# Kernel tuning notes

Hardware: AMD Instinct MI355X
Metric: run time of the kernel (lower is better)

The kernel has to match this reference:

```python
import jax, jax.numpy as jnp
import numpy as np

N = 50000      # nodes
E = 800000     # edges (before self loops)
F_IN = 128
HID = 32
HEADS = 4
OUT_DIM = 1
NEG_SLOPE = 0.2


def gat_conv(x, edge_src, edge_dst, W, a_src, a_dst, bias):
    """PyG GATConv (concat=True, self-loops already appended to edge lists).
    x: [N, Fin], W: [Fin, H*D], a_src/a_dst: [H, D], bias: [H*D]."""
    H, D = a_src.shape
    h = (x @ W).reshape(N, H, D)                      # [N, H, D]
    alpha_src = jnp.einsum('nhd,hd->nh', h, a_src)    # [N, H]
    alpha_dst = jnp.einsum('nhd,hd->nh', h, a_dst)    # [N, H]
    e = alpha_src[edge_src] + alpha_dst[edge_dst]     # [Et, H]
    e = jnp.where(e > 0, e, NEG_SLOPE * e)            # leaky_relu(0.2)
    # softmax over edges grouped by destination node
    m = jax.ops.segment_max(e, edge_dst, num_segments=N)  # [N, H]
    e = jnp.exp(e - jax.lax.stop_gradient(m)[edge_dst])
    s = jax.ops.segment_sum(e, edge_dst, num_segments=N)  # [N, H]
    alpha = e / (s[edge_dst] + 1e-16)                 # [Et, H]
    msg = h[edge_src] * alpha[:, :, None]             # [Et, H, D]
    out = jax.ops.segment_sum(msg, edge_dst, num_segments=N)  # [N, H, D]
    return out.reshape(N, H * D) + bias


def setup_inputs() -> dict:
    key = jax.random.key(0)
    ks = jax.random.split(key, 16)
    HD = HEADS * HID
    def glorot(k, shape, fan_in):
        return jax.random.normal(k, shape, dtype=jnp.float32) / np.sqrt(fan_in)
    inp = {
        'x': jax.random.normal(ks[0], (N, F_IN), dtype=jnp.float32),
        'edge_index': jax.random.randint(ks[1], (2, E), 0, N, dtype=jnp.int64 if jax.config.jax_enable_x64 else jnp.int32),
        'W1': glorot(ks[2], (F_IN, HD), F_IN),
        'a_src1': glorot(ks[3], (HEADS, HID), HID),
        'a_dst1': glorot(ks[4], (HEADS, HID), HID),
        'b1': jnp.zeros((HD,), dtype=jnp.float32),
        'W2': glorot(ks[5], (HD, HD), HD),
        'a_src2': glorot(ks[6], (HEADS, HID), HID),
        'a_dst2': glorot(ks[7], (HEADS, HID), HID),
        'b2': jnp.zeros((HD,), dtype=jnp.float32),
        'Wc1': glorot(ks[8], (HD, HID), HD),
        'bc1': jnp.zeros((HID,), dtype=jnp.float32),
        'Wc2': glorot(ks[9], (HID, OUT_DIM), HID),
        'bc2': jnp.zeros((OUT_DIM,), dtype=jnp.float32),
    }
    return inp


def reference(x, edge_index, W1, a_src1, a_dst1, b1, W2, a_src2, a_dst2, b2,
              Wc1, bc1, Wc2, bc2):
    # PyG add_self_loops=True: append (i -> i) for every node
    loops = jnp.arange(N, dtype=edge_index.dtype)
    src = jnp.concatenate([edge_index[0], loops])
    dst = jnp.concatenate([edge_index[1], loops])
    h = gat_conv(x, src, dst, W1, a_src1, a_dst1, b1)
    h = jax.nn.relu(h)
    h = gat_conv(h, src, dst, W2, a_src2, a_dst2, b2)
    h = jax.nn.relu(h)
    # classifier (dropout is identity at eval)
    h = h @ Wc1 + bc1
    h = h @ Wc2 + bc2
    return jax.nn.sigmoid(h)
```

## Files before the change

kernel.cpp:

```cpp
#include <hip/hip_runtime.h>
#include <hip/hip_bf16.h>
#include <math.h>

#define NEG_SLOPE 0.2f

__device__ __forceinline__ unsigned short f2bf(float f) {
    unsigned int u = __float_as_uint(f);
    u = (u + 0x7fffu + ((u >> 16) & 1u)) >> 16;
    return (unsigned short)u;
}
__device__ __forceinline__ float bflo(unsigned int p) {
    return __uint_as_float(p << 16);
}
__device__ __forceinline__ float bfhi(unsigned int p) {
    return __uint_as_float(p & 0xffff0000u);
}

__global__ __launch_bounds__(256) void gemm_alpha_kernel(
    const float* __restrict__ X, const float* __restrict__ W,
    const float* __restrict__ a_src, const float* __restrict__ a_dst,
    unsigned short* __restrict__ Hb, float* __restrict__ as_out,
    float* __restrict__ ad_out, int N)
{
    __shared__ float xt[64 * 128];
    int n0 = blockIdx.x * 64;
    int t  = threadIdx.x;

    {
        const float4* src = (const float4*)(X + (size_t)n0 * 128);
        float4* dst = (float4*)xt;
        int rows = N - n0; if (rows > 64) rows = 64;
        int maxv = rows * 32;
        #pragma unroll
        for (int i = 0; i < 8; ++i) {
            int idx = t + i * 256;
            int g = idx < maxv ? idx : maxv - 1;
            dst[idx] = src[g];
        }
    }
    __syncthreads();

    int rg = t >> 5;
    int c  = t & 31;
    int j0 = c * 4;

    float acc[8][4];
    #pragma unroll
    for (int rr = 0; rr < 8; ++rr)
        { acc[rr][0]=0.f; acc[rr][1]=0.f; acc[rr][2]=0.f; acc[rr][3]=0.f; }

    #pragma unroll 2
    for (int k = 0; k < 128; ++k) {
        float4 w = *(const float4*)(W + k * 128 + j0);
        #pragma unroll
        for (int rr = 0; rr < 8; ++rr) {
            float xv = xt[(rg + rr * 8) * 128 + k];
            acc[rr][0] = fmaf(xv, w.x, acc[rr][0]);
            acc[rr][1] = fmaf(xv, w.y, acc[rr][1]);
            acc[rr][2] = fmaf(xv, w.z, acc[rr][2]);
            acc[rr][3] = fmaf(xv, w.w, acc[rr][3]);
        }
    }

    float4 asv = *(const float4*)(a_src + j0);
    float4 adv = *(const float4*)(a_dst + j0);
    int head = c >> 3;
    int wlane = (c & 7) == 0;

    #pragma unroll
    for (int rr = 0; rr < 8; ++rr) {
        float b0 = acc[rr][0], b1 = acc[rr][1], b2 = acc[rr][2], b3 = acc[rr][3];
        int row = n0 + rg + rr * 8;
        bool valid = row < N;
        if (valid) {
            unsigned int lo = (unsigned int)f2bf(b0) | ((unsigned int)f2bf(b1) << 16);
            unsigned int hi = (unsigned int)f2bf(b2) | ((unsigned int)f2bf(b3) << 16);
            *(uint2*)(Hb + (size_t)row * 128 + j0) = make_uint2(lo, hi);
        }
        float ps = b0*asv.x + b1*asv.y + b2*asv.z + b3*asv.w;
        float pd = b0*adv.x + b1*adv.y + b2*adv.z + b3*adv.w;
        ps += __shfl_xor(ps, 1, 64); pd += __shfl_xor(pd, 1, 64);
        ps += __shfl_xor(ps, 2, 64); pd += __shfl_xor(pd, 2, 64);
        ps += __shfl_xor(ps, 4, 64); pd += __shfl_xor(pd, 4, 64);
        if (wlane && valid) {
            as_out[row * 4 + head] = ps;
            ad_out[row * 4 + head] = pd;
        }
    }
}

__global__ __launch_bounds__(256) void zero_int_kernel(int* __restrict__ p, int n)
{
    int i = blockIdx.x * 256 + threadIdx.x;
    if (i < n) p[i] = 0;
}

__global__ __launch_bounds__(256) void count_rank_kernel(
    const int* __restrict__ edst, int E, int Et,
    int* __restrict__ cnt, int* __restrict__ rank)
{
    int e = blockIdx.x * 256 + threadIdx.x;
    if (e >= Et) return;
    int d = (e < E) ? edst[e] : (e - E);
    rank[e] = atomicAdd(&cnt[d], 1);
}

__global__ __launch_bounds__(256) void pos_kernel(
    const int* __restrict__ edst, int E, int Et,
    const int* __restrict__ offs, int* __restrict__ rank)
{
    int e = blockIdx.x * 256 + threadIdx.x;
    if (e >= Et) return;
    int d = (e < E) ? edst[e] : (e - E);
    rank[e] = offs[d] + rank[e];
}

__global__ __launch_bounds__(256) void scan_block_kernel(
    const int* __restrict__ in, int* __restrict__ out,
    int* __restrict__ bsum, int n)
{
    __shared__ int sh[256];
    int i = blockIdx.x * 256 + threadIdx.x;
    int v = (i < n) ? in[i] : 0;
    sh[threadIdx.x] = v;
    __syncthreads();
    #pragma unroll
    for (int off = 1; off < 256; off <<= 1) {
        int t = 0;
        if (threadIdx.x >= off) t = sh[threadIdx.x - off];
        __syncthreads();
        if (threadIdx.x >= off) sh[threadIdx.x] += t;
        __syncthreads();
    }
    if (i < n) out[i] = sh[threadIdx.x] - v;
    if (threadIdx.x == 255) bsum[blockIdx.x] = sh[255];
}

__global__ __launch_bounds__(256) void scan_add_kernel(
    int* __restrict__ offs, const int* __restrict__ bsum, int n)
{
    int i = blockIdx.x * 256 + threadIdx.x;
    if (i < n) offs[i] += bsum[blockIdx.x];
}

__global__ __launch_bounds__(256) void fill_kernel(
    const int* __restrict__ esrc, int E, int Et, int N,
    const int* __restrict__ offs, const int* __restrict__ pos,
    int* __restrict__ csr, int S)
{
    int slice = blockIdx.x >> 3;
    int l8 = blockIdx.x & 7;
    if (slice >= S) return;
    int rlo = (int)(((long long)N * l8) >> 3);
    int rhi = (int)(((long long)N * (l8 + 1)) >> 3);
    int csrLo = offs[rlo];
    int csrHi = (rhi < N) ? offs[rhi] : Et;
    int e0 = (int)((long long)Et * slice / S);
    int e1 = (int)((long long)Et * (slice + 1) / S);
    for (int e = e0 + threadIdx.x; e < e1; e += 256) {
        int p = pos[e];
        if (p >= csrLo && p < csrHi)
            csr[p] = (e < E) ? esrc[e] : (e - E);
    }
}

__global__ __launch_bounds__(128) void cls_vec_kernel(
    const float* __restrict__ Wc1, const float* __restrict__ bc1,
    const float* __restrict__ Wc2, const float* __restrict__ bc2,
    float* __restrict__ v)
{
    int i = threadIdx.x;
    float acc = 0.f;
    #pragma unroll
    for (int j = 0; j < 32; ++j)
        acc = fmaf(Wc1[i * 32 + j], Wc2[j], acc);
    v[i] = acc;
    if (i == 0) {
        float c = bc2[0];
        for (int j = 0; j < 32; ++j)
            c = fmaf(bc1[j], Wc2[j], c);
        v[128] = c;
    }
}

__global__ __launch_bounds__(256) void gat_fused_kernel(
    const unsigned short* __restrict__ Hb, const int* __restrict__ csr,
    const int* __restrict__ offs, const int* __restrict__ cnt,
    const float* __restrict__ as, const float* __restrict__ ad,
    const float* __restrict__ bias, float* __restrict__ out, int N,
    const float* __restrict__ v, float* __restrict__ dcls, int docls)
{
    __shared__ float wtab[4 * 256];
    __shared__ int   stab[4 * 64];

    int t = threadIdx.x;
    int wv = t >> 6;
    int g  = (t >> 4) & 3;
    int q  = t & 15;
    int d = blockIdx.x * 16 + (t >> 4);
    if (d >= N) return;
    int start = offs[d];
    int deg = cnt[d];
    float4 adv = *(const float4*)(ad + d * 4);
    int h = q >> 2;
    int f0 = q * 8;

    float m0 = -INFINITY, m1 = -INFINITY, m2 = -INFINITY, m3 = -INFINITY;
    float s0 = 0.f, s1 = 0.f, s2 = 0.f, s3 = 0.f;
    float acc0=0.f,acc1=0.f,acc2=0.f,acc3=0.f,acc4=0.f,acc5=0.f,acc6=0.f,acc7=0.f;

    const float* wbase = wtab + wv * 256 + g * 4 + h;
    const int*   sbase = stab + wv * 64 + g * 16;

    for (int c0 = 0; c0 < deg; c0 += 16) {
        int rem = deg - c0;
        int len = rem < 16 ? rem : 16;
        bool valid = q < len;
        int sidx = valid ? csr[start + c0 + q] : 0;
        float4 av = *(const float4*)(as + sidx * 4);
        float e0 = av.x + adv.x; e0 = e0 > 0.f ? e0 : NEG_SLOPE * e0;
        float e1 = av.y + adv.y; e1 = e1 > 0.f ? e1 : NEG_SLOPE * e1;
        float e2 = av.z + adv.z; e2 = e2 > 0.f ? e2 : NEG_SLOPE * e2;
        float e3 = av.w + adv.w; e3 = e3 > 0.f ? e3 : NEG_SLOPE * e3;
        if (!valid) { e0 = e1 = e2 = e3 = -INFINITY; }

        float c0m = e0, c1m = e1, c2m = e2, c3m = e3;
        #pragma unroll
        for (int off = 8; off; off >>= 1) {
            c0m = fmaxf(c0m, __shfl_xor(c0m, off, 64));
            c1m = fmaxf(c1m, __shfl_xor(c1m, off, 64));
            c2m = fmaxf(c2m, __shfl_xor(c2m, off, 64));
            c3m = fmaxf(c3m, __shfl_xor(c3m, off, 64));
        }
        float nm0 = fmaxf(m0, c0m), nm1 = fmaxf(m1, c1m);
        float nm2 = fmaxf(m2, c2m), nm3 = fmaxf(m3, c3m);
        float r0 = __expf(m0 - nm0), r1 = __expf(m1 - nm1);
        float r2 = __expf(m2 - nm2), r3 = __expf(m3 - nm3);
        m0 = nm0; m1 = nm1; m2 = nm2; m3 = nm3;

        float w0 = valid ? __expf(e0 - m0) : 0.f;
        float w1 = valid ? __expf(e1 - m1) : 0.f;
        float w2 = valid ? __expf(e2 - m2) : 0.f;
        float w3 = valid ? __expf(e3 - m3) : 0.f;

        float t0 = w0, t1 = w1, t2 = w2, t3 = w3;
        #pragma unroll
        for (int off = 8; off; off >>= 1) {
            t0 += __shfl_xor(t0, off, 64);
            t1 += __shfl_xor(t1, off, 64);
            t2 += __shfl_xor(t2, off, 64);
            t3 += __shfl_xor(t3, off, 64);
        }
        s0 = s0 * r0 + t0; s1 = s1 * r1 + t1;
        s2 = s2 * r2 + t2; s3 = s3 * r3 + t3;
        float rs = h == 0 ? r0 : (h == 1 ? r1 : (h == 2 ? r2 : r3));
        acc0 *= rs; acc1 *= rs; acc2 *= rs; acc3 *= rs;
        acc4 *= rs; acc5 *= rs; acc6 *= rs; acc7 *= rs;

        ((float4*)wtab)[wv * 64 + q * 4 + g] = make_float4(w0, w1, w2, w3);
        stab[wv * 64 + g * 16 + q] = sidx;

        int kk = 0;
        for (; kk + 4 <= len; kk += 4) {
            int sk0 = sbase[kk+0], sk1 = sbase[kk+1];
            int sk2 = sbase[kk+2], sk3 = sbase[kk+3];
            float wa = wbase[(kk+0)*16], wb = wbase[(kk+1)*16];
            float wc = wbase[(kk+2)*16], wd = wbase[(kk+3)*16];
            uint4 p0 = *(const uint4*)(Hb + (size_t)sk0 * 128 + f0);
            uint4 p1 = *(const uint4*)(Hb + (size_t)sk1 * 128 + f0);
            uint4 p2 = *(const uint4*)(Hb + (size_t)sk2 * 128 + f0);
            uint4 p3 = *(const uint4*)(Hb + (size_t)sk3 * 128 + f0);
            acc0 = fmaf(wa, bflo(p0.x), acc0); acc1 = fmaf(wa, bfhi(p0.x), acc1);
            acc2 = fmaf(wa, bflo(p0.y), acc2); acc3 = fmaf(wa, bfhi(p0.y), acc3);
            acc4 = fmaf(wa, bflo(p0.z), acc4); acc5 = fmaf(wa, bfhi(p0.z), acc5);
            acc6 = fmaf(wa, bflo(p0.w), acc6); acc7 = fmaf(wa, bfhi(p0.w), acc7);
            acc0 = fmaf(wb, bflo(p1.x), acc0); acc1 = fmaf(wb, bfhi(p1.x), acc1);
            acc2 = fmaf(wb, bflo(p1.y), acc2); acc3 = fmaf(wb, bfhi(p1.y), acc3);
            acc4 = fmaf(wb, bflo(p1.z), acc4); acc5 = fmaf(wb, bfhi(p1.z), acc5);
            acc6 = fmaf(wb, bflo(p1.w), acc6); acc7 = fmaf(wb, bfhi(p1.w), acc7);
            acc0 = fmaf(wc, bflo(p2.x), acc0); acc1 = fmaf(wc, bfhi(p2.x), acc1);
            acc2 = fmaf(wc, bflo(p2.y), acc2); acc3 = fmaf(wc, bfhi(p2.y), acc3);
            acc4 = fmaf(wc, bflo(p2.z), acc4); acc5 = fmaf(wc, bfhi(p2.z), acc5);
            acc6 = fmaf(wc, bflo(p2.w), acc6); acc7 = fmaf(wc, bfhi(p2.w), acc7);
            acc0 = fmaf(wd, bflo(p3.x), acc0); acc1 = fmaf(wd, bfhi(p3.x), acc1);
            acc2 = fmaf(wd, bflo(p3.y), acc2); acc3 = fmaf(wd, bfhi(p3.y), acc3);
            acc4 = fmaf(wd, bflo(p3.z), acc4); acc5 = fmaf(wd, bfhi(p3.z), acc5);
            acc6 = fmaf(wd, bflo(p3.w), acc6); acc7 = fmaf(wd, bfhi(p3.w), acc7);
        }
        for (; kk < len; ++kk) {
            int sk = sbase[kk];
            float wk = wbase[kk*16];
            uint4 p = *(const uint4*)(Hb + (size_t)sk * 128 + f0);
            acc0 = fmaf(wk, bflo(p.x), acc0); acc1 = fmaf(wk, bfhi(p.x), acc1);
            acc2 = fmaf(wk, bflo(p.y), acc2); acc3 = fmaf(wk, bfhi(p.y), acc3);
            acc4 = fmaf(wk, bflo(p.z), acc4); acc5 = fmaf(wk, bfhi(p.z), acc5);
            acc6 = fmaf(wk, bflo(p.w), acc6); acc7 = fmaf(wk, bfhi(p.w), acc7);
        }
    }

    float sh = h == 0 ? s0 : (h == 1 ? s1 : (h == 2 ? s2 : s3));
    float inv = 1.f / (sh + 1e-16f);
    float4 bA = *(const float4*)(bias + f0);
    float4 bB = *(const float4*)(bias + f0 + 4);
    float o0 = fmaxf(acc0 * inv + bA.x, 0.f);
    float o1 = fmaxf(acc1 * inv + bA.y, 0.f);
    float o2 = fmaxf(acc2 * inv + bA.z, 0.f);
    float o3 = fmaxf(acc3 * inv + bA.w, 0.f);
    float o4 = fmaxf(acc4 * inv + bB.x, 0.f);
    float o5 = fmaxf(acc5 * inv + bB.y, 0.f);
    float o6 = fmaxf(acc6 * inv + bB.z, 0.f);
    float o7 = fmaxf(acc7 * inv + bB.w, 0.f);

    if (!docls) {
        *(float4*)(out + (size_t)d * 128 + f0)     = make_float4(o0, o1, o2, o3);
        *(float4*)(out + (size_t)d * 128 + f0 + 4) = make_float4(o4, o5, o6, o7);
    } else {
        float4 vA = *(const float4*)(v + f0);
        float4 vB = *(const float4*)(v + f0 + 4);
        float part = o0*vA.x + o1*vA.y + o2*vA.z + o3*vA.w
                   + o4*vB.x + o5*vB.y + o6*vB.z + o7*vB.w;
        part += __shfl_xor(part, 1, 64);
        part += __shfl_xor(part, 2, 64);
        part += __shfl_xor(part, 4, 64);
        part += __shfl_xor(part, 8, 64);
        if (q == 0)
            dcls[d] = 1.0f / (1.0f + __expf(-(part + v[128])));
    }
}

extern "C" void kernel_launch(void* const* d_in, const int* in_sizes, int n_in,
                              void* d_out, int out_size, void* d_ws, size_t ws_size,
                              hipStream_t stream)
{
    const float* x      = (const float*)d_in[0];
    const int*   eidx   = (const int*)d_in[1];
    const float* W1     = (const float*)d_in[2];
    const float* a_src1 = (const float*)d_in[3];
    const float* a_dst1 = (const float*)d_in[4];
    const float* b1     = (const float*)d_in[5];
    const float* W2     = (const float*)d_in[6];
    const float* a_src2 = (const float*)d_in[7];
    const float* a_dst2 = (const float*)d_in[8];
    const float* b2     = (const float*)d_in[9];
    const float* Wc1    = (const float*)d_in[10];
    const float* bc1    = (const float*)d_in[11];
    const float* Wc2    = (const float*)d_in[12];
    const float* bc2    = (const float*)d_in[13];

    int N  = in_sizes[0] / 128;
    int E  = in_sizes[1] / 2;
    int Et = E + N;
    const int* esrc = eidx;
    const int* edst = eidx + E;

    char* wsb = (char*)d_ws;
    unsigned short* Hb = (unsigned short*)wsb;  wsb += (size_t)N * 128 * 2;
    float*  f1_buf = (float*)wsb;   wsb += (size_t)N * 128 * 4;
    float*  as_buf = (float*)wsb;   wsb += (size_t)N * 4 * 4;
    float*  ad_buf = (float*)wsb;   wsb += (size_t)N * 4 * 4;
    int*    cnt    = (int*)wsb;     wsb += (size_t)N * 4;
    int*    offs   = (int*)wsb;     wsb += (size_t)N * 4;
    int*    bsum   = (int*)wsb;     wsb += 512 * 4;
    int*    csr    = (int*)wsb;     wsb += (size_t)Et * 4;
    int*    rank   = (int*)wsb;     wsb += (size_t)Et * 4;
    float*  vcls   = (float*)wsb;   wsb += 132 * 4;

    int nbN = (N + 255) / 256;
    int nbE = (Et + 255) / 256;
    int gemmBlocks = (N + 63) / 64;
    int S = 512;

    zero_int_kernel<<<nbN, 256, 0, stream>>>(cnt, N);
    count_rank_kernel<<<nbE, 256, 0, stream>>>(edst, E, Et, cnt, rank);
    scan_block_kernel<<<nbN, 256, 0, stream>>>(cnt, offs, bsum, N);
    scan_block_kernel<<<1, 256, 0, stream>>>(bsum, bsum, &bsum[300], nbN);
    scan_add_kernel<<<nbN, 256, 0, stream>>>(offs, bsum, N);
    pos_kernel<<<nbE, 256, 0, stream>>>(edst, E, Et, offs, rank);
    cls_vec_kernel<<<1, 128, 0, stream>>>(Wc1, bc1, Wc2, bc2, vcls);
    fill_kernel<<<S * 8, 256, 0, stream>>>(esrc, E, Et, N, offs, rank, csr, S);

    gemm_alpha_kernel<<<gemmBlocks, 256, 0, stream>>>(x, W1, a_src1, a_dst1,
                                                      Hb, as_buf, ad_buf, N);
    gat_fused_kernel<<<(N + 15) / 16, 256, 0, stream>>>(Hb, csr, offs, cnt,
        as_buf, ad_buf, b1, f1_buf, N, vcls, (float*)d_out, 0);
    gemm_alpha_kernel<<<gemmBlocks, 256, 0, stream>>>(f1_buf, W2, a_src2, a_dst2,
                                                      Hb, as_buf, ad_buf, N);
    gat_fused_kernel<<<(N + 15) / 16, 256, 0, stream>>>(Hb, csr, offs, cnt,
        as_buf, ad_buf, b2, f1_buf, N, vcls, (float*)d_out, 1);
}
```

Measured before the change: 310.7 us.

## Process 64-edge chunks per destination and unroll the gather loop by eight

Each destination's 16-lane group now handles up to 64 incoming edges per iteration, with every lane scoring four edges. The score max and sum are combined locally before the cross-lane shuffles. This cuts the number of online-softmax rescale and shuffle rounds for typical degrees near 17. The gather loop now issues eight bf16 row loads before accumulating, to keep more memory requests in flight. The cost is more registers for the edge scores and loaded rows, plus a larger shared-memory table, which may lower occupancy.

```diff
diff --git a/kernel.cpp b/kernel.cpp
--- a/kernel.cpp
+++ b/kernel.cpp
@@ -190,14 +190,14 @@
     const float* __restrict__ bias, float* __restrict__ out, int N,
     const float* __restrict__ v, float* __restrict__ dcls, int docls)
 {
-    __shared__ float wtab[4 * 256];
-    __shared__ int   stab[4 * 64];
+    __shared__ float wtab[4][64][16];
+    __shared__ int   stab[4][4][64];
 
     int t = threadIdx.x;
     int wv = t >> 6;
     int g  = (t >> 4) & 3;
     int q  = t & 15;
-    int d = blockIdx.x * 16 + (t >> 4);
+    int d = blockIdx.x * 16 + wv * 4 + g;
     if (d >= N) return;
     int start = offs[d];
     int deg = cnt[d];
@@ -209,22 +209,32 @@
     float s0 = 0.f, s1 = 0.f, s2 = 0.f, s3 = 0.f;
     float acc0=0.f,acc1=0.f,acc2=0.f,acc3=0.f,acc4=0.f,acc5=0.f,acc6=0.f,acc7=0.f;
 
-    const float* wbase = wtab + wv * 256 + g * 4 + h;
-    const int*   sbase = stab + wv * 64 + g * 16;
-
-    for (int c0 = 0; c0 < deg; c0 += 16) {
+    const float* wb = &wtab[wv][0][g * 4 + h];
+    const int*   sb = &stab[wv][g][0];
+
+    for (int c0 = 0; c0 < deg; c0 += 64) {
         int rem = deg - c0;
-        int len = rem < 16 ? rem : 16;
-        bool valid = q < len;
-        int sidx = valid ? csr[start + c0 + q] : 0;
-        float4 av = *(const float4*)(as + sidx * 4);
-        float e0 = av.x + adv.x; e0 = e0 > 0.f ? e0 : NEG_SLOPE * e0;
-        float e1 = av.y + adv.y; e1 = e1 > 0.f ? e1 : NEG_SLOPE * e1;
-        float e2 = av.z + adv.z; e2 = e2 > 0.f ? e2 : NEG_SLOPE * e2;
-        float e3 = av.w + adv.w; e3 = e3 > 0.f ? e3 : NEG_SLOPE * e3;
-        if (!valid) { e0 = e1 = e2 = e3 = -INFINITY; }
-
-        float c0m = e0, c1m = e1, c2m = e2, c3m = e3;
+        int len = rem < 64 ? rem : 64;
+
+        int   sidx[4];
+        float ev[4][4];
+        #pragma unroll
+        for (int i = 0; i < 4; ++i) {
+            int j = q * 4 + i;
+            bool valid = j < len;
+            sidx[i] = valid ? csr[start + c0 + j] : 0;
+            float4 av = *(const float4*)(as + sidx[i] * 4);
+            float e0 = av.x + adv.x; e0 = e0 > 0.f ? e0 : NEG_SLOPE * e0;
+            float e1 = av.y + adv.y; e1 = e1 > 0.f ? e1 : NEG_SLOPE * e1;
+            float e2 = av.z + adv.z; e2 = e2 > 0.f ? e2 : NEG_SLOPE * e2;
+            float e3 = av.w + adv.w; e3 = e3 > 0.f ? e3 : NEG_SLOPE * e3;
+            if (!valid) { e0 = e1 = e2 = e3 = -INFINITY; }
+            ev[i][0] = e0; ev[i][1] = e1; ev[i][2] = e2; ev[i][3] = e3;
+        }
+        float c0m = fmaxf(fmaxf(ev[0][0], ev[1][0]), fmaxf(ev[2][0], ev[3][0]));
+        float c1m = fmaxf(fmaxf(ev[0][1], ev[1][1]), fmaxf(ev[2][1], ev[3][1]));
+        float c2m = fmaxf(fmaxf(ev[0][2], ev[1][2]), fmaxf(ev[2][2], ev[3][2]));
+        float c3m = fmaxf(fmaxf(ev[0][3], ev[1][3]), fmaxf(ev[2][3], ev[3][3]));
         #pragma unroll
         for (int off = 8; off; off >>= 1) {
             c0m = fmaxf(c0m, __shfl_xor(c0m, off, 64));
@@ -238,12 +248,19 @@
         float r2 = __expf(m2 - nm2), r3 = __expf(m3 - nm3);
         m0 = nm0; m1 = nm1; m2 = nm2; m3 = nm3;
 
-        float w0 = valid ? __expf(e0 - m0) : 0.f;
-        float w1 = valid ? __expf(e1 - m1) : 0.f;
-        float w2 = valid ? __expf(e2 - m2) : 0.f;
-        float w3 = valid ? __expf(e3 - m3) : 0.f;
-
-        float t0 = w0, t1 = w1, t2 = w2, t3 = w3;
+        float t0 = 0.f, t1 = 0.f, t2 = 0.f, t3 = 0.f;
+        #pragma unroll
+        for (int i = 0; i < 4; ++i) {
+            int j = q * 4 + i;
+            bool valid = j < len;
+            float w0 = valid ? __expf(ev[i][0] - m0) : 0.f;
+            float w1 = valid ? __expf(ev[i][1] - m1) : 0.f;
+            float w2 = valid ? __expf(ev[i][2] - m2) : 0.f;
+            float w3 = valid ? __expf(ev[i][3] - m3) : 0.f;
+            t0 += w0; t1 += w1; t2 += w2; t3 += w3;
+            *(float4*)&wtab[wv][j][g * 4] = make_float4(w0, w1, w2, w3);
+            stab[wv][g][j] = sidx[i];
+        }
         #pragma unroll
         for (int off = 8; off; off >>= 1) {
             t0 += __shfl_xor(t0, off, 64);
@@ -257,44 +274,36 @@
         acc0 *= rs; acc1 *= rs; acc2 *= rs; acc3 *= rs;
         acc4 *= rs; acc5 *= rs; acc6 *= rs; acc7 *= rs;
 
-        ((float4*)wtab)[wv * 64 + q * 4 + g] = make_float4(w0, w1, w2, w3);
-        stab[wv * 64 + g * 16 + q] = sidx;
-
         int kk = 0;
-        for (; kk + 4 <= len; kk += 4) {
-            int sk0 = sbase[kk+0], sk1 = sbase[kk+1];
-            int sk2 = sbase[kk+2], sk3 = sbase[kk+3];
-            float wa = wbase[(kk+0)*16], wb = wbase[(kk+1)*16];
-            float wc = wbase[(kk+2)*16], wd = wbase[(kk+3)*16];
-            uint4 p0 = *(const uint4*)(Hb + (size_t)sk0 * 128 + f0);
-            uint4 p1 = *(const uint4*)(Hb + (size_t)sk1 * 128 + f0);
-            uint4 p2 = *(const uint4*)(Hb + (size_t)sk2 * 128 + f0);
-            uint4 p3 = *(const uint4*)(Hb + (size_t)sk3 * 128 + f0);
-            acc0 = fmaf(wa, bflo(p0.x), acc0); acc1 = fmaf(wa, bfhi(p0.x), acc1);
-            acc2 = fmaf(wa, bflo(p0.y), acc2); acc3 = fmaf(wa, bfhi(p0.y), acc3);
-            acc4 = fmaf(wa, bflo(p0.z), acc4); acc5 = fmaf(wa, bfhi(p0.z), acc5);
-            acc6 = fmaf(wa, bflo(p0.w), acc6); acc7 = fmaf(wa, bfhi(p0.w), acc7);
-            acc0 = fmaf(wb, bflo(p1.x), acc0); acc1 = fmaf(wb, bfhi(p1.x), acc1);
-            acc2 = fmaf(wb, bflo(p1.y), acc2); acc3 = fmaf(wb, bfhi(p1.y), acc3);
-            acc4 = fmaf(wb, bflo(p1.z), acc4); acc5 = fmaf(wb, bfhi(p1.z), acc5);
-            acc6 = fmaf(wb, bflo(p1.w), acc6); acc7 = fmaf(wb, bfhi(p1.w), acc7);
-            acc0 = fmaf(wc, bflo(p2.x), acc0); acc1 = fmaf(wc, bfhi(p2.x), acc1);
-            acc2 = fmaf(wc, bflo(p2.y), acc2); acc3 = fmaf(wc, bfhi(p2.y), acc3);
-            acc4 = fmaf(wc, bflo(p2.z), acc4); acc5 = fmaf(wc, bfhi(p2.z), acc5);
-            acc6 = fmaf(wc, bflo(p2.w), acc6); acc7 = fmaf(wc, bfhi(p2.w), acc7);
-            acc0 = fmaf(wd, bflo(p3.x), acc0); acc1 = fmaf(wd, bfhi(p3.x), acc1);
-            acc2 = fmaf(wd, bflo(p3.y), acc2); acc3 = fmaf(wd, bfhi(p3.y), acc3);
-            acc4 = fmaf(wd, bflo(p3.z), acc4); acc5 = fmaf(wd, bfhi(p3.z), acc5);
-            acc6 = fmaf(wd, bflo(p3.w), acc6); acc7 = fmaf(wd, bfhi(p3.w), acc7);
+        for (; kk + 8 <= len; kk += 8) {
+            uint4 p[8];
+            float wk[8];
+            #pragma unroll
+            for (int i = 0; i < 8; ++i) {
+                int sk = sb[kk + i];
+                wk[i] = wb[(kk + i) * 16];
+                p[i] = *(const uint4*)(Hb + (size_t)sk * 128 + f0);
+            }
+            #pragma unroll
+            for (int i = 0; i < 8; ++i) {
+                acc0 = fmaf(wk[i], bflo(p[i].x), acc0);
+                acc1 = fmaf(wk[i], bfhi(p[i].x), acc1);
+                acc2 = fmaf(wk[i], bflo(p[i].y), acc2);
+                acc3 = fmaf(wk[i], bfhi(p[i].y), acc3);
+                acc4 = fmaf(wk[i], bflo(p[i].z), acc4);
+                acc5 = fmaf(wk[i], bfhi(p[i].z), acc5);
+                acc6 = fmaf(wk[i], bflo(p[i].w), acc6);
+                acc7 = fmaf(wk[i], bfhi(p[i].w), acc7);
+            }
         }
         for (; kk < len; ++kk) {
-            int sk = sbase[kk];
-            float wk = wbase[kk*16];
+            int sk = sb[kk];
+            float wkk = wb[kk * 16];
             uint4 p = *(const uint4*)(Hb + (size_t)sk * 128 + f0);
-            acc0 = fmaf(wk, bflo(p.x), acc0); acc1 = fmaf(wk, bfhi(p.x), acc1);
-            acc2 = fmaf(wk, bflo(p.y), acc2); acc3 = fmaf(wk, bfhi(p.y), acc3);
-            acc4 = fmaf(wk, bflo(p.z), acc4); acc5 = fmaf(wk, bfhi(p.z), acc5);
-            acc6 = fmaf(wk, bflo(p.w), acc6); acc7 = fmaf(wk, bfhi(p.w), acc7);
+            acc0 = fmaf(wkk, bflo(p.x), acc0); acc1 = fmaf(wkk, bfhi(p.x), acc1);
+            acc2 = fmaf(wkk, bflo(p.y), acc2); acc3 = fmaf(wkk, bfhi(p.y), acc3);
+            acc4 = fmaf(wkk, bflo(p.z), acc4); acc5 = fmaf(wkk, bfhi(p.z), acc5);
+            acc6 = fmaf(wkk, bflo(p.w), acc6); acc7 = fmaf(wkk, bfhi(p.w), acc7);
         }
     }
 
```

After: 313.3 us. About the same (+0.8%).
